# Optimization experiments

Measured on AMD Instinct MI355X. Metric: run time of the kernel, lower is better.

## Reference

```python
import jax, jax.numpy as jnp
import numpy as np

N, D, L, OUT, E = 50000, 64, 3, 16, 800000


def setup_inputs() -> dict:
    key = jax.random.key(0)
    ks = jax.random.split(key, 7)
    F = jax.random.normal(ks[0], (N, D), dtype=jnp.float32)
    src = jax.random.randint(ks[1], (E,), 0, N, dtype=jnp.int32)
    dst = jax.random.randint(ks[2], (E,), 0, N, dtype=jnp.int32)
    gcn_w = jax.random.normal(ks[3], (L, D, D), dtype=jnp.float32) / np.float32(np.sqrt(D))
    gcn_b = jnp.zeros((L, D), dtype=jnp.float32)
    fc_w = jax.random.normal(ks[4], (OUT, N * D), dtype=jnp.float32) / np.float32(np.sqrt(N * D))
    fc_b = jnp.zeros((OUT,), dtype=jnp.float32)
    return {"F": F, "src": src, "dst": dst, "gcn_w": gcn_w, "gcn_b": gcn_b,
            "fc_w": fc_w, "fc_b": fc_b}


def reference(F, src, dst, gcn_w, gcn_b, fc_w, fc_b):
    n = F.shape[0]
    # dgl.add_self_loop: append a self edge for every node
    loops = jnp.arange(n, dtype=src.dtype)
    s = jnp.concatenate([src, loops])
    d = jnp.concatenate([dst, loops])
    ones = jnp.ones(s.shape[0], dtype=F.dtype)
    deg_out = jax.ops.segment_sum(ones, s, num_segments=n)  # out-degree of src
    deg_in = jax.ops.segment_sum(ones, d, num_segments=n)   # in-degree of dst
    # self loops guarantee deg >= 1
    norm_src = deg_out ** -0.5
    norm_dst = deg_in ** -0.5
    x = F
    for i in range(gcn_w.shape[0]):
        h = x * norm_src[:, None]                              # [N, D]
        agg = jax.ops.segment_sum(h[s], d, num_segments=n)     # SpMM gather-scatter
        x = (agg * norm_dst[:, None]) @ gcn_w[i] + gcn_b[i]    # GraphConv norm='both'
        x = jax.nn.relu(x)
    flat = jax.nn.relu(x.reshape(-1))                          # Flatten(start_dim=0) + ReLU
    return fc_w @ flat + fc_b                                  # [OUT]
```

## Files before the change

kernel.cpp:

```cpp
#include <hip/hip_runtime.h>
#include <cstdint>

#define Nn 50000
#define Dd 64
#define Ee 800000
#define NBLK 196
#define EBLK (Ee/256)
#define FC_BLOCKS 512
#define ND4 (Nn*Dd/4)
#define H0BLK (ND4/256 + 1)
#define NDTOT ((size_t)Nn * 64)

__device__ __forceinline__ float relu_f(float v){ return v > 0.f ? v : 0.f; }

__device__ __forceinline__ unsigned short f2bf(float f){
    unsigned u = __float_as_uint(f);
    u += 0x7fffu + ((u >> 16) & 1u);
    return (unsigned short)(u >> 16);
}
__device__ __forceinline__ void add_bf8(float* a, uint4 u){
    a[0] += __uint_as_float(u.x << 16);
    a[1] += __uint_as_float(u.x & 0xffff0000u);
    a[2] += __uint_as_float(u.y << 16);
    a[3] += __uint_as_float(u.y & 0xffff0000u);
    a[4] += __uint_as_float(u.z << 16);
    a[5] += __uint_as_float(u.z & 0xffff0000u);
    a[6] += __uint_as_float(u.w << 16);
    a[7] += __uint_as_float(u.w & 0xffff0000u);
}
__device__ __forceinline__ int rowidx(unsigned e, unsigned end, const unsigned* __restrict__ csr){
    unsigned ec = e < (Ee - 1u) ? e : (Ee - 1u);
    int idx = (int)csr[ec];
    return (e < end) ? idx : Nn;
}

__global__ __launch_bounds__(256) void k_degree(const int* __restrict__ src, const int* __restrict__ dst,
                                                unsigned* __restrict__ dout, unsigned* __restrict__ din){
    int e = blockIdx.x * 256 + threadIdx.x;
    if (e < Ee){
        atomicAdd(&dout[src[e]], 1u);
        atomicAdd(&din[dst[e]], 1u);
    }
}

__global__ __launch_bounds__(256) void k_blocksum(const unsigned* __restrict__ din, const unsigned* __restrict__ dout,
                                                  unsigned* __restrict__ bsum,
                                                  float* __restrict__ ns, float* __restrict__ nd){
    __shared__ unsigned s[256];
    int t = threadIdx.x; int i = blockIdx.x * 256 + t;
    unsigned v = (i < Nn) ? din[i] : 0u;
    s[t] = v;
    if (i < Nn){
        ns[i] = rsqrtf((float)(dout[i] + 1u));
        nd[i] = rsqrtf((float)(v + 1u));
    }
    __syncthreads();
    for (int off = 128; off > 0; off >>= 1){ if (t < off) s[t] += s[t + off]; __syncthreads(); }
    if (t == 0) bsum[blockIdx.x] = s[0];
}

__global__ __launch_bounds__(256) void k_offsets(const unsigned* __restrict__ din, const unsigned* __restrict__ bsum,
                                                 unsigned* __restrict__ offsets, unsigned* __restrict__ cursor){
    __shared__ unsigned s[256];
    __shared__ unsigned sboff, stot;
    int t = threadIdx.x; int bid = blockIdx.x;
    unsigned bv = (t < NBLK) ? bsum[t] : 0u;
    s[t] = bv; __syncthreads();
    for (int off = 1; off < 256; off <<= 1){
        unsigned add = (t >= off) ? s[t - off] : 0u;
        __syncthreads();
        s[t] += add;
        __syncthreads();
    }
    if (t == 0)   sboff = (bid > 0) ? s[bid - 1] : 0u;
    if (t == 255) stot  = s[255];
    __syncthreads();
    unsigned boff = sboff;
    int i = bid * 256 + t;
    unsigned v = (i < Nn) ? din[i] : 0u;
    s[t] = v; __syncthreads();
    for (int off = 1; off < 256; off <<= 1){
        unsigned add = (t >= off) ? s[t - off] : 0u;
        __syncthreads();
        s[t] += add;
        __syncthreads();
    }
    if (i < Nn){
        unsigned val = s[t] - v + boff;
        offsets[i] = val;
        cursor[i]  = val;
    }
    if (bid == 0 && t == 0) offsets[Nn] = stot;
}

__global__ __launch_bounds__(256) void k_fill_h0(const int* __restrict__ src, const int* __restrict__ dst,
                                                 unsigned* __restrict__ cursor, unsigned* __restrict__ csr,
                                                 const float* __restrict__ x, const float* __restrict__ ns,
                                                 unsigned short* __restrict__ hA, unsigned short* __restrict__ hB){
    int b = blockIdx.x;
    if (b < EBLK){
        int e = b * 256 + threadIdx.x;
        unsigned pos = atomicAdd(&cursor[dst[e]], 1u);
        csr[pos] = (unsigned)src[e];
    } else {
        int i = (b - EBLK) * 256 + threadIdx.x;
        if (i < ND4){
            const float4* x4 = (const float4*)x;
            float s = ns[i >> 4];
            float4 v = x4[i];
            ushort4 o;
            o.x = f2bf(v.x * s); o.y = f2bf(v.y * s);
            o.z = f2bf(v.z * s); o.w = f2bf(v.w * s);
            ((ushort4*)hA)[i] = o;
        } else {
            int j = i - ND4;
            if (j < 16){
                ushort4 z = make_ushort4(0, 0, 0, 0);
                ((ushort4*)hA)[ND4 + j] = z;
                ((ushort4*)hB)[ND4 + j] = z;
            }
        }
    }
}

__global__ __launch_bounds__(256) void k_gather(const unsigned short* __restrict__ h,
                                                const unsigned* __restrict__ offsets,
                                                const unsigned* __restrict__ csr, const float* __restrict__ nd,
                                                float* __restrict__ agg){
    int v = blockIdx.x * 4 + (threadIdx.x >> 6);
    int lane = threadIdx.x & 63;
    int slot = lane >> 3;
    int sub  = lane & 7;
    const uint4* h16 = (const uint4*)h;

    unsigned beg = offsets[v], end = offsets[v + 1];
    unsigned e0 = beg + slot;

    int i0 = rowidx(e0,      end, csr);
    int i1 = rowidx(e0 + 8,  end, csr);
    int i2 = rowidx(e0 + 16, end, csr);
    int i3 = rowidx(e0 + 24, end, csr);
    uint4 u0 = h16[(size_t)i0 * 8 + sub];
    uint4 u1 = h16[(size_t)i1 * 8 + sub];
    uint4 u2 = h16[(size_t)i2 * 8 + sub];
    uint4 u3 = h16[(size_t)i3 * 8 + sub];

    float acc[8];
    #pragma unroll
    for (int i = 0; i < 8; i++) acc[i] = 0.f;
    if (slot == 0) add_bf8(acc, h16[(size_t)v * 8 + sub]);
    add_bf8(acc, u0);
    add_bf8(acc, u1);
    add_bf8(acc, u2);
    add_bf8(acc, u3);

    for (unsigned e = e0 + 32; e < end; e += 8){
        add_bf8(acc, h16[(size_t)((int)csr[e]) * 8 + sub]);
    }

    #pragma unroll
    for (int i = 0; i < 8; i++) acc[i] += __shfl_xor(acc[i], 8, 64);
    #pragma unroll
    for (int i = 0; i < 8; i++) acc[i] += __shfl_xor(acc[i], 16, 64);
    #pragma unroll
    for (int i = 0; i < 8; i++) acc[i] += __shfl_xor(acc[i], 32, 64);

    if (slot == 0){
        float s = nd[v];
        float4* aggp = (float4*)agg;
        aggp[(size_t)v * 16 + sub * 2 + 0] = make_float4(acc[0] * s, acc[1] * s, acc[2] * s, acc[3] * s);
        aggp[(size_t)v * 16 + sub * 2 + 1] = make_float4(acc[4] * s, acc[5] * s, acc[6] * s, acc[7] * s);
    }
}

__global__ __launch_bounds__(256) void k_gemm(const float* __restrict__ agg, const float* __restrict__ W,
                                              const float* __restrict__ bias, const float* __restrict__ ns,
                                              void* __restrict__ xout, int bf16_prescale_out){
    __shared__ float As[64 * 65];
    __shared__ float Ws[64 * 64];
    int t = threadIdx.x;
    int m_base = blockIdx.x * 64;
    const float4* W4   = (const float4*)W;
    float4* Ws4        = (float4*)Ws;
    const float4* agg4 = (const float4*)agg;
    #pragma unroll
    for (int i = 0; i < 4; i++){
        int g = t + 256 * i;
        Ws4[g] = W4[g];
        int m = g >> 4, q = g & 15;
        int node = m_base + m;
        float4 v = make_float4(0.f, 0.f, 0.f, 0.f);
        if (node < Nn) v = agg4[node * 16 + q];
        float* dp = &As[m * 65 + q * 4];
        dp[0] = v.x; dp[1] = v.y; dp[2] = v.z; dp[3] = v.w;
    }
    __syncthreads();
    int tm = t >> 4, tn = t & 15;
    float acc[4][4];
    #pragma unroll
    for (int i = 0; i < 4; i++)
        #pragma unroll
        for (int j = 0; j < 4; j++) acc[i][j] = 0.f;
    #pragma unroll 4
    for (int k = 0; k < 64; k++){
        float4 w = *(const float4*)&Ws[k * 64 + tn * 4];
        float a[4];
        #pragma unroll
        for (int i = 0; i < 4; i++) a[i] = As[(tm * 4 + i) * 65 + k];
        #pragma unroll
        for (int i = 0; i < 4; i++){
            acc[i][0] += a[i] * w.x;
            acc[i][1] += a[i] * w.y;
            acc[i][2] += a[i] * w.z;
            acc[i][3] += a[i] * w.w;
        }
    }
    float4 b4 = ((const float4*)bias)[tn];
    #pragma unroll
    for (int i = 0; i < 4; i++){
        int node = m_base + tm * 4 + i;
        if (node < Nn){
            float4 r;
            r.x = relu_f(acc[i][0] + b4.x);
            r.y = relu_f(acc[i][1] + b4.y);
            r.z = relu_f(acc[i][2] + b4.z);
            r.w = relu_f(acc[i][3] + b4.w);
            if (bf16_prescale_out){
                float s = ns[node];
                ushort4 o;
                o.x = f2bf(r.x * s); o.y = f2bf(r.y * s);
                o.z = f2bf(r.z * s); o.w = f2bf(r.w * s);
                ((ushort4*)xout)[node * 16 + tn] = o;
            } else {
                ((float4*)xout)[node * 16 + tn] = r;
            }
        }
    }
}

__global__ __launch_bounds__(256) void k_fc(const float* __restrict__ fcw, const float* __restrict__ x,
                                            float* __restrict__ partials){
    int t = threadIdx.x;
    const float4* x4 = (const float4*)x;
    const float4* w4 = (const float4*)fcw;
    float p[16];
    #pragma unroll
    for (int o = 0; o < 16; o++) p[o] = 0.f;
    for (int i = blockIdx.x * 256 + t; i < ND4; i += FC_BLOCKS * 256){
        float4 xv = x4[i];
        #pragma unroll
        for (int o = 0; o < 16; o++){
            float4 wv = w4[(size_t)o * ND4 + i];
            p[o] += wv.x * xv.x + wv.y * xv.y + wv.z * xv.z + wv.w * xv.w;
        }
    }
    #pragma unroll
    for (int o = 0; o < 16; o++){
        for (int off = 32; off > 0; off >>= 1) p[o] += __shfl_down(p[o], off, 64);
    }
    __shared__ float red[4][16];
    int lane = t & 63, wid = t >> 6;
    if (lane == 0){
        #pragma unroll
        for (int o = 0; o < 16; o++) red[wid][o] = p[o];
    }
    __syncthreads();
    if (t < 16) partials[blockIdx.x * 16 + t] = red[0][t] + red[1][t] + red[2][t] + red[3][t];
}

__global__ __launch_bounds__(256) void k_fc2(const float* __restrict__ partials, const float* __restrict__ fcb,
                                             float* __restrict__ out){
    __shared__ float red[256];
    int t = threadIdx.x; int o = t & 15, j0 = t >> 4;
    float s = 0.f;
    for (int j = j0; j < FC_BLOCKS; j += 16) s += partials[j * 16 + o];
    red[t] = s; __syncthreads();
    for (int off = 128; off >= 16; off >>= 1){ if (t < off) red[t] += red[t + off]; __syncthreads(); }
    if (t < 16) out[t] = red[t] + fcb[t];
}

extern "C" void kernel_launch(void* const* d_in, const int* in_sizes, int n_in,
                              void* d_out, int out_size, void* d_ws, size_t ws_size,
                              hipStream_t stream) {
    const float* F     = (const float*)d_in[0];
    const int*   src   = (const int*)d_in[1];
    const int*   dst   = (const int*)d_in[2];
    const float* gcn_w = (const float*)d_in[3];
    const float* gcn_b = (const float*)d_in[4];
    const float* fc_w  = (const float*)d_in[5];
    const float* fc_b  = (const float*)d_in[6];
    float* out = (float*)d_out;

    char* wsp = (char*)d_ws;
    auto alloc = [&](size_t bytes) -> char* {
        char* p = wsp;
        wsp += (bytes + 255) & ~size_t(255);
        return p;
    };
    unsigned* deg      = (unsigned*)alloc(2 * Nn * 4);
    unsigned* deg_out_ = deg;
    unsigned* deg_in_  = deg + Nn;
    unsigned* offsets  = (unsigned*)alloc((Nn + 1) * 4);
    unsigned* cursor   = (unsigned*)alloc(Nn * 4);
    unsigned* bsum     = (unsigned*)alloc(256 * 4);
    unsigned* csr      = (unsigned*)alloc(Ee * 4);
    float* norm_src    = (float*)alloc(Nn * 4);
    float* norm_dst    = (float*)alloc(Nn * 4);
    float* partials    = (float*)alloc(FC_BLOCKS * 16 * 4);
    unsigned short* hA = (unsigned short*)alloc((NDTOT + 64) * 2);
    unsigned short* hB = (unsigned short*)alloc((NDTOT + 64) * 2);
    float* aggb        = (float*)alloc(NDTOT * 4);
    float* xf          = (float*)alloc(NDTOT * 4);

    hipMemsetAsync(deg, 0, 2 * Nn * 4, stream);

    k_degree  <<<EBLK, 256, 0, stream>>>(src, dst, deg_out_, deg_in_);
    k_blocksum<<<NBLK, 256, 0, stream>>>(deg_in_, deg_out_, bsum, norm_src, norm_dst);
    k_offsets <<<NBLK, 256, 0, stream>>>(deg_in_, bsum, offsets, cursor);
    k_fill_h0 <<<EBLK + H0BLK, 256, 0, stream>>>(src, dst, cursor, csr, F, norm_src, hA, hB);

    int nblk_gemm = (Nn + 63) / 64;
    k_gather<<<Nn / 4, 256, 0, stream>>>(hA, offsets, csr, norm_dst, aggb);
    k_gemm<<<nblk_gemm, 256, 0, stream>>>(aggb, gcn_w + 0 * 4096, gcn_b + 0 * 64, norm_src, hB, 1);
    k_gather<<<Nn / 4, 256, 0, stream>>>(hB, offsets, csr, norm_dst, aggb);
    k_gemm<<<nblk_gemm, 256, 0, stream>>>(aggb, gcn_w + 1 * 4096, gcn_b + 1 * 64, norm_src, hA, 1);
    k_gather<<<Nn / 4, 256, 0, stream>>>(hA, offsets, csr, norm_dst, aggb);
    k_gemm<<<nblk_gemm, 256, 0, stream>>>(aggb, gcn_w + 2 * 4096, gcn_b + 2 * 64, norm_src, xf, 0);

    k_fc <<<FC_BLOCKS, 256, 0, stream>>>(fc_w, xf, partials);
    k_fc2<<<1, 256, 0, stream>>>(partials, fc_b, out);
}
```

Before: 534.2 us.

## Fuse final FC matvec into last GEMM epilogue, vectorize degree count, trim gather prefetch

The last GCN GEMM no longer writes an fp32 node-feature buffer. It multiplies its ReLU output directly against fc_w and writes per-block partials, which removes the separate k_fc kernel and the xf round trip through memory. The degree kernel now loads four edge indices per thread with int4 loads. The gather kernel prefetches only two neighbor rows unconditionally and guards the third and fourth behind degree checks, cutting wasted loads for low-degree nodes at the cost of some branching. The bf16 output stores were also split into scalar ushort writes, which may produce less efficient stores.

```diff
diff --git a/kernel.cpp b/kernel.cpp
--- a/kernel.cpp
+++ b/kernel.cpp
@@ -6,7 +6,8 @@
 #define Ee 800000
 #define NBLK 196
 #define EBLK (Ee/256)
-#define FC_BLOCKS 512
+#define E4BLK ((Ee/4 + 255)/256)
+#define GBLK ((Nn + 63)/64)
 #define ND4 (Nn*Dd/4)
 #define H0BLK (ND4/256 + 1)
 #define NDTOT ((size_t)Nn * 64)
@@ -36,10 +37,14 @@
 
 __global__ __launch_bounds__(256) void k_degree(const int* __restrict__ src, const int* __restrict__ dst,
                                                 unsigned* __restrict__ dout, unsigned* __restrict__ din){
-    int e = blockIdx.x * 256 + threadIdx.x;
-    if (e < Ee){
-        atomicAdd(&dout[src[e]], 1u);
-        atomicAdd(&din[dst[e]], 1u);
+    int e4 = blockIdx.x * 256 + threadIdx.x;
+    if (e4 < Ee/4){
+        int4 s4 = ((const int4*)src)[e4];
+        int4 d4 = ((const int4*)dst)[e4];
+        atomicAdd(&dout[s4.x], 1u); atomicAdd(&dout[s4.y], 1u);
+        atomicAdd(&dout[s4.z], 1u); atomicAdd(&dout[s4.w], 1u);
+        atomicAdd(&din[d4.x], 1u);  atomicAdd(&din[d4.y], 1u);
+        atomicAdd(&din[d4.z], 1u);  atomicAdd(&din[d4.w], 1u);
     }
 }
 
@@ -134,16 +139,13 @@
     const uint4* h16 = (const uint4*)h;
 
     unsigned beg = offsets[v], end = offsets[v + 1];
+    unsigned deg = end - beg;
     unsigned e0 = beg + slot;
 
-    int i0 = rowidx(e0,      end, csr);
-    int i1 = rowidx(e0 + 8,  end, csr);
-    int i2 = rowidx(e0 + 16, end, csr);
-    int i3 = rowidx(e0 + 24, end, csr);
+    int i0 = rowidx(e0,     end, csr);
+    int i1 = rowidx(e0 + 8, end, csr);
     uint4 u0 = h16[(size_t)i0 * 8 + sub];
     uint4 u1 = h16[(size_t)i1 * 8 + sub];
-    uint4 u2 = h16[(size_t)i2 * 8 + sub];
-    uint4 u3 = h16[(size_t)i3 * 8 + sub];
 
     float acc[8];
     #pragma unroll
@@ -151,11 +153,17 @@
     if (slot == 0) add_bf8(acc, h16[(size_t)v * 8 + sub]);
     add_bf8(acc, u0);
     add_bf8(acc, u1);
-    add_bf8(acc, u2);
-    add_bf8(acc, u3);
-
-    for (unsigned e = e0 + 32; e < end; e += 8){
-        add_bf8(acc, h16[(size_t)((int)csr[e]) * 8 + sub]);
+
+    if (deg > 16u){
+        int i2 = rowidx(e0 + 16, end, csr);
+        add_bf8(acc, h16[(size_t)i2 * 8 + sub]);
+    }
+    if (deg > 24u){
+        int i3 = rowidx(e0 + 24, end, csr);
+        add_bf8(acc, h16[(size_t)i3 * 8 + sub]);
+        for (unsigned e = e0 + 32; e < end; e += 8){
+            add_bf8(acc, h16[(size_t)((int)csr[e]) * 8 + sub]);
+        }
     }
 
     #pragma unroll
@@ -175,9 +183,12 @@
 
 __global__ __launch_bounds__(256) void k_gemm(const float* __restrict__ agg, const float* __restrict__ W,
                                               const float* __restrict__ bias, const float* __restrict__ ns,
-                                              void* __restrict__ xout, int bf16_prescale_out){
+                                              unsigned short* __restrict__ hout,
+                                              const float* __restrict__ fcw, float* __restrict__ partials,
+                                              int fc_mode){
     __shared__ float As[64 * 65];
     __shared__ float Ws[64 * 64];
+    __shared__ float red[4][16];
     int t = threadIdx.x;
     int m_base = blockIdx.x * 64;
     const float4* W4   = (const float4*)W;
@@ -216,56 +227,62 @@
         }
     }
     float4 b4 = ((const float4*)bias)[tn];
-    #pragma unroll
-    for (int i = 0; i < 4; i++){
-        int node = m_base + tm * 4 + i;
-        if (node < Nn){
-            float4 r;
-            r.x = relu_f(acc[i][0] + b4.x);
-            r.y = relu_f(acc[i][1] + b4.y);
-            r.z = relu_f(acc[i][2] + b4.z);
-            r.w = relu_f(acc[i][3] + b4.w);
-            if (bf16_prescale_out){
+
+    if (!fc_mode){
+        #pragma unroll
+        for (int i = 0; i < 4; i++){
+            int node = m_base + tm * 4 + i;
+            if (node < Nn){
+                float4 r;
+                r.x = relu_f(acc[i][0] + b4.x);
+                r.y = relu_f(acc[i][1] + b4.y);
+                r.z = relu_f(acc[i][2] + b4.z);
+                r.w = relu_f(acc[i][3] + b4.w);
                 float s = ns[node];
                 ushort4 o;
                 o.x = f2bf(r.x * s); o.y = f2bf(r.y * s);
                 o.z = f2bf(r.z * s); o.w = f2bf(r.w * s);
-                ((ushort4*)xout)[node * 16 + tn] = o;
-            } else {
-                ((float4*)xout)[node * 16 + tn] = r;
+                hout[(size_t)node * 64 + tn * 4 + 0] = o.x;
+                hout[(size_t)node * 64 + tn * 4 + 1] = o.y;
+                hout[(size_t)node * 64 + tn * 4 + 2] = o.z;
+                hout[(size_t)node * 64 + tn * 4 + 3] = o.w;
             }
         }
-    }
-}
-
-__global__ __launch_bounds__(256) void k_fc(const float* __restrict__ fcw, const float* __restrict__ x,
-                                            float* __restrict__ partials){
-    int t = threadIdx.x;
-    const float4* x4 = (const float4*)x;
-    const float4* w4 = (const float4*)fcw;
-    float p[16];
-    #pragma unroll
-    for (int o = 0; o < 16; o++) p[o] = 0.f;
-    for (int i = blockIdx.x * 256 + t; i < ND4; i += FC_BLOCKS * 256){
-        float4 xv = x4[i];
+    } else {
+        float p[16];
+        #pragma unroll
+        for (int o = 0; o < 16; o++) p[o] = 0.f;
+        const float4* w4 = (const float4*)fcw;
+        #pragma unroll
+        for (int i = 0; i < 4; i++){
+            int node = m_base + tm * 4 + i;
+            if (node < Nn){
+                float4 r;
+                r.x = relu_f(acc[i][0] + b4.x);
+                r.y = relu_f(acc[i][1] + b4.y);
+                r.z = relu_f(acc[i][2] + b4.z);
+                r.w = relu_f(acc[i][3] + b4.w);
+                size_t base = (size_t)node * 16 + tn;
+                #pragma unroll
+                for (int o = 0; o < 16; o++){
+                    float4 wv = w4[(size_t)o * ND4 + base];
+                    p[o] += wv.x * r.x + wv.y * r.y + wv.z * r.z + wv.w * r.w;
+                }
+            }
+        }
+        int lane = t & 63, wid = t >> 6;
         #pragma unroll
         for (int o = 0; o < 16; o++){
-            float4 wv = w4[(size_t)o * ND4 + i];
-            p[o] += wv.x * xv.x + wv.y * xv.y + wv.z * xv.z + wv.w * xv.w;
-        }
-    }
-    #pragma unroll
-    for (int o = 0; o < 16; o++){
-        for (int off = 32; off > 0; off >>= 1) p[o] += __shfl_down(p[o], off, 64);
-    }
-    __shared__ float red[4][16];
-    int lane = t & 63, wid = t >> 6;
-    if (lane == 0){
-        #pragma unroll
-        for (int o = 0; o < 16; o++) red[wid][o] = p[o];
-    }
-    __syncthreads();
-    if (t < 16) partials[blockIdx.x * 16 + t] = red[0][t] + red[1][t] + red[2][t] + red[3][t];
+            #pragma unroll
+            for (int off = 32; off > 0; off >>= 1) p[o] += __shfl_down(p[o], off, 64);
+        }
+        if (lane == 0){
+            #pragma unroll
+            for (int o = 0; o < 16; o++) red[wid][o] = p[o];
+        }
+        __syncthreads();
+        if (t < 16) partials[blockIdx.x * 16 + t] = red[0][t] + red[1][t] + red[2][t] + red[3][t];
+    }
 }
 
 __global__ __launch_bounds__(256) void k_fc2(const float* __restrict__ partials, const float* __restrict__ fcb,
@@ -273,7 +290,7 @@
     __shared__ float red[256];
     int t = threadIdx.x; int o = t & 15, j0 = t >> 4;
     float s = 0.f;
-    for (int j = j0; j < FC_BLOCKS; j += 16) s += partials[j * 16 + o];
+    for (int j = j0; j < GBLK; j += 16) s += partials[j * 16 + o];
     red[t] = s; __syncthreads();
     for (int off = 128; off >= 16; off >>= 1){ if (t < off) red[t] += red[t + off]; __syncthreads(); }
     if (t < 16) out[t] = red[t] + fcb[t];
@@ -306,27 +323,24 @@
     unsigned* csr      = (unsigned*)alloc(Ee * 4);
     float* norm_src    = (float*)alloc(Nn * 4);
     float* norm_dst    = (float*)alloc(Nn * 4);
-    float* partials    = (float*)alloc(FC_BLOCKS * 16 * 4);
+    float* partials    = (float*)alloc(GBLK * 16 * 4);
     unsigned short* hA = (unsigned short*)alloc((NDTOT + 64) * 2);
     unsigned short* hB = (unsigned short*)alloc((NDTOT + 64) * 2);
     float* aggb        = (float*)alloc(NDTOT * 4);
-    float* xf          = (float*)alloc(NDTOT * 4);
 
     hipMemsetAsync(deg, 0, 2 * Nn * 4, stream);
 
-    k_degree  <<<EBLK, 256, 0, stream>>>(src, dst, deg_out_, deg_in_);
+    k_degree  <<<E4BLK, 256, 0, stream>>>(src, dst, deg_out_, deg_in_);
     k_blocksum<<<NBLK, 256, 0, stream>>>(deg_in_, deg_out_, bsum, norm_src, norm_dst);
     k_offsets <<<NBLK, 256, 0, stream>>>(deg_in_, bsum, offsets, cursor);
     k_fill_h0 <<<EBLK + H0BLK, 256, 0, stream>>>(src, dst, cursor, csr, F, norm_src, hA, hB);
 
-    int nblk_gemm = (Nn + 63) / 64;
     k_gather<<<Nn / 4, 256, 0, stream>>>(hA, offsets, csr, norm_dst, aggb);
-    k_gemm<<<nblk_gemm, 256, 0, stream>>>(aggb, gcn_w + 0 * 4096, gcn_b + 0 * 64, norm_src, hB, 1);
+    k_gemm<<<GBLK, 256, 0, stream>>>(aggb, gcn_w + 0 * 4096, gcn_b + 0 * 64, norm_src, hB, nullptr, nullptr, 0);
     k_gather<<<Nn / 4, 256, 0, stream>>>(hB, offsets, csr, norm_dst, aggb);
-    k_gemm<<<nblk_gemm, 256, 0, stream>>>(aggb, gcn_w + 1 * 4096, gcn_b + 1 * 64, norm_src, hA, 1);
+    k_gemm<<<GBLK, 256, 0, stream>>>(aggb, gcn_w + 1 * 4096, gcn_b + 1 * 64, norm_src, hA, nullptr, nullptr, 0);
     k_gather<<<Nn / 4, 256, 0, stream>>>(hA, offsets, csr, norm_dst, aggb);
-    k_gemm<<<nblk_gemm, 256, 0, stream>>>(aggb, gcn_w + 2 * 4096, gcn_b + 2 * 64, norm_src, xf, 0);
-
-    k_fc <<<FC_BLOCKS, 256, 0, stream>>>(fc_w, xf, partials);
+    k_gemm<<<GBLK, 256, 0, stream>>>(aggb, gcn_w + 2 * 4096, gcn_b + 2 * 64, norm_src, nullptr, fc_w, partials, 1);
+
     k_fc2<<<1, 256, 0, stream>>>(partials, fc_b, out);
 }
```

Measured after the change: 544.9 us. About the same (+2.0%).
